# Optimization experiments

Measured on AMD Instinct MI355X. Metric: run time of the kernel, lower is better.

The kernel has to match this reference:

```python
import jax, jax.numpy as jnp
import numpy as np

LD, LU, N, D_IN, D_OUT, K = 16384, 65536, 8, 256, 128, 3


def setup_inputs() -> dict:
    key = jax.random.key(0)
    ks = jax.random.split(key, 7)
    down_features = jax.random.normal(ks[0], (LD, N, D_IN), dtype=jnp.float32)
    up_features = jax.random.normal(ks[1], (LU, N, D_OUT), dtype=jnp.float32)
    idx = jax.random.randint(ks[2], (LU, N, K), 0, LD, dtype=jnp.int32)
    W1 = jax.random.normal(ks[3], (D_IN, D_OUT), dtype=jnp.float32) / np.sqrt(D_IN)
    b1 = jnp.zeros((D_OUT,), dtype=jnp.float32)
    W2 = jax.random.normal(ks[4], (D_OUT, D_OUT), dtype=jnp.float32) / np.sqrt(D_OUT)
    b2 = jnp.zeros((D_OUT,), dtype=jnp.float32)
    return {"down_features": down_features, "up_features": up_features, "idx": idx,
            "W1": W1, "b1": b1, "W2": W2, "b2": b2}


def reference(down_features, up_features, idx, W1, b1, W2, b2):
    # MLP: Linear(d, d_out) -> ReLU -> Linear(d_out, d_out), applied per point
    h = jax.nn.relu(jnp.einsum("lnd,de->lne", down_features, W1) + b1)
    h = jnp.einsum("lnd,de->lne", h, W2) + b2            # (Ld, N, Du)
    # KNN upsample: gather K neighbors per upsampled point, average, residual add
    n = jnp.arange(h.shape[1])[None, :, None]            # (1, N, 1) batch index
    gathered = h[idx, n, :]                              # (Lu, N, K, Du)
    up = up_features + gathered.mean(axis=2)             # (Lu, N, Du)
    return up
```

## Files before the change

kernel.cpp:

```cpp
#include <hip/hip_runtime.h>

#define LD_   16384
#define LU_   65536
#define N_    8
#define DIN   256
#define DOUT  128
#define K_    3
#define M_    (LD_ * N_)

typedef short bf16x8 __attribute__((ext_vector_type(8)));
typedef float f32x4  __attribute__((ext_vector_type(4)));
typedef unsigned int u32x2 __attribute__((ext_vector_type(2)));

__device__ __forceinline__ unsigned short f2bf(float f) {
    unsigned int x = __float_as_uint(f);
    x += 0x7fffu + ((x >> 16) & 1u);
    return (unsigned short)(x >> 16);
}

__device__ __forceinline__ bf16x8 ld_bf16x8(const unsigned short* p) {
    const short4 lo = *(const short4*)p;
    const short4 hi = *(const short4*)(p + 4);
    bf16x8 r = {lo.x, lo.y, lo.z, lo.w, hi.x, hi.y, hi.z, hi.w};
    return r;
}

#define W1_STRIDE 264
#define W2_STRIDE 132
#define H1_STRIDE 132

__global__ __launch_bounds__(512, 2) void knn_mlp_mfma(
    const float* __restrict__ down, const float* __restrict__ W1,
    const float* __restrict__ b1,   const float* __restrict__ W2,
    const float* __restrict__ b2,   unsigned short* __restrict__ h)
{
    __shared__ unsigned short sW1t[DOUT * W1_STRIDE];
    __shared__ unsigned short sW2t[DOUT * W2_STRIDE];
    __shared__ unsigned short sH[8][16 * H1_STRIDE];
    __shared__ float sB1[DOUT], sB2[DOUT];

    const int tid  = threadIdx.x;
    const int wave = tid >> 6, lane = tid & 63;
    const int lm = lane & 15, lg = lane >> 4;

    const int row0 = blockIdx.x * 512 + wave * 16;
    const float* dbase = down + (size_t)(row0 + lm) * DIN + lg * 8;

    float4 raw[16];
    #pragma unroll
    for (int k = 0; k < 8; ++k) {
        raw[2 * k]     = *(const float4*)(dbase + k * 32);
        raw[2 * k + 1] = *(const float4*)(dbase + k * 32 + 4);
    }

    #pragma unroll
    for (int it = 0; it < 16; ++it) {
        const int fid = it * 512 + tid;
        const int k = fid >> 5, n4 = (fid & 31) * 4;
        const float4 w = ((const float4*)W1)[fid];
        sW1t[(n4 + 0) * W1_STRIDE + k] = f2bf(w.x);
        sW1t[(n4 + 1) * W1_STRIDE + k] = f2bf(w.y);
        sW1t[(n4 + 2) * W1_STRIDE + k] = f2bf(w.z);
        sW1t[(n4 + 3) * W1_STRIDE + k] = f2bf(w.w);
    }
    #pragma unroll
    for (int it = 0; it < 8; ++it) {
        const int fid = it * 512 + tid;
        const int k = fid >> 5, n4 = (fid & 31) * 4;
        const float4 w = ((const float4*)W2)[fid];
        sW2t[(n4 + 0) * W2_STRIDE + k] = f2bf(w.x);
        sW2t[(n4 + 1) * W2_STRIDE + k] = f2bf(w.y);
        sW2t[(n4 + 2) * W2_STRIDE + k] = f2bf(w.z);
        sW2t[(n4 + 3) * W2_STRIDE + k] = f2bf(w.w);
    }
    if (tid < 32)                 ((float4*)sB1)[tid]      = ((const float4*)b1)[tid];
    else if (tid < 64)            ((float4*)sB2)[tid - 32] = ((const float4*)b2)[tid - 32];
    __syncthreads();

    unsigned short* hw = sH[wave];

    #pragma unroll
    for (int pass = 0; pass < 4; ++pass) {
        const int chunk = row0 + pass * 128;

        bf16x8 A[8];
        #pragma unroll
        for (int k = 0; k < 8; ++k) {
            const float4 r0 = raw[2 * k], r1 = raw[2 * k + 1];
            const bf16x8 a = {(short)f2bf(r0.x), (short)f2bf(r0.y), (short)f2bf(r0.z), (short)f2bf(r0.w),
                              (short)f2bf(r1.x), (short)f2bf(r1.y), (short)f2bf(r1.z), (short)f2bf(r1.w)};
            A[k] = a;
        }

        if (pass < 3) {
            const float* dp = dbase + (size_t)(pass + 1) * 128 * DIN;
            #pragma unroll
            for (int k = 0; k < 8; ++k) {
                raw[2 * k]     = *(const float4*)(dp + k * 32);
                raw[2 * k + 1] = *(const float4*)(dp + k * 32 + 4);
            }
        }

        f32x4 acc[8];
        #pragma unroll
        for (int nt = 0; nt < 8; ++nt) acc[nt] = (f32x4){0.f, 0.f, 0.f, 0.f};
        #pragma unroll
        for (int k = 0; k < 8; ++k) {
            const int koff = k * 32 + lg * 8;
            #pragma unroll
            for (int nt = 0; nt < 8; ++nt) {
                const bf16x8 Wf = ld_bf16x8(&sW1t[(nt * 16 + lm) * W1_STRIDE + koff]);
                acc[nt] = __builtin_amdgcn_mfma_f32_16x16x32_bf16(Wf, A[k], acc[nt], 0, 0, 0);
            }
        }

        #pragma unroll
        for (int nt = 0; nt < 8; ++nt) {
            const float4 bq = *(const float4*)&sB1[nt * 16 + lg * 4];
            ushort4 st;
            st.x = f2bf(fmaxf(acc[nt][0] + bq.x, 0.0f));
            st.y = f2bf(fmaxf(acc[nt][1] + bq.y, 0.0f));
            st.z = f2bf(fmaxf(acc[nt][2] + bq.z, 0.0f));
            st.w = f2bf(fmaxf(acc[nt][3] + bq.w, 0.0f));
            *(ushort4*)&hw[lm * H1_STRIDE + nt * 16 + lg * 4] = st;
        }
        asm volatile("s_waitcnt lgkmcnt(0)" ::: "memory");

        f32x4 acc2[8];
        #pragma unroll
        for (int nt = 0; nt < 8; ++nt) acc2[nt] = (f32x4){0.f, 0.f, 0.f, 0.f};
        #pragma unroll
        for (int ks = 0; ks < 4; ++ks) {
            const int koff = ks * 32 + lg * 8;
            const bf16x8 Bh = ld_bf16x8(&hw[lm * H1_STRIDE + koff]);
            #pragma unroll
            for (int nt = 0; nt < 8; ++nt) {
                const bf16x8 Wf = ld_bf16x8(&sW2t[(nt * 16 + lm) * W2_STRIDE + koff]);
                acc2[nt] = __builtin_amdgcn_mfma_f32_16x16x32_bf16(Wf, Bh, acc2[nt], 0, 0, 0);
            }
        }

        #pragma unroll
        for (int nt = 0; nt < 8; ++nt) {
            const float4 bq = *(const float4*)&sB2[nt * 16 + lg * 4];
            ushort4 st;
            st.x = f2bf(acc2[nt][0] + bq.x);
            st.y = f2bf(acc2[nt][1] + bq.y);
            st.z = f2bf(acc2[nt][2] + bq.z);
            st.w = f2bf(acc2[nt][3] + bq.w);
            *(ushort4*)&h[(size_t)(chunk + lm) * DOUT + nt * 16 + lg * 4] = st;
        }
    }
}

__global__ __launch_bounds__(256) void knn_gather(
    const float* __restrict__ up, const int* __restrict__ idx,
    const unsigned int* __restrict__ h32, float* __restrict__ out)
{
    const int wave = threadIdx.x >> 6, lane = threadIdx.x & 63;
    const int half = lane >> 5, lih = lane & 31;
    const long long wid  = (long long)blockIdx.x * 4 + wave;
    const long long base = wid * 64;

    const int* ip = idx + (base + lane) * 3;
    const int mi0 = ip[0], mi1 = ip[1], mi2 = ip[2];

    const u32x2* hg   = (const u32x2*)h32;
    const f32x4* upv  = (const f32x4*)up;
    f32x4*       outv = (f32x4*)out;

    #pragma unroll
    for (int gb = 0; gb < 8; ++gb) {
        u32x2 ga[4][3];
        f32x4 uu[4];
        int   pp[4];
        #pragma unroll
        for (int u = 0; u < 4; ++u) {
            const int p = (gb * 4 + u) * 2 + half;
            pp[u] = p;
            const int i0 = __shfl(mi0, p);
            const int i1 = __shfl(mi1, p);
            const int i2 = __shfl(mi2, p);
            const int n  = p & 7;
            ga[u][0] = hg[(unsigned)(i0 * 8 + n) * 32u + lih];
            ga[u][1] = hg[(unsigned)(i1 * 8 + n) * 32u + lih];
            ga[u][2] = hg[(unsigned)(i2 * 8 + n) * 32u + lih];
            uu[u] = __builtin_nontemporal_load(&upv[(base + p) * 32 + lih]);
        }
        #pragma unroll
        for (int u = 0; u < 4; ++u) {
            float s0 = 0.f, s1 = 0.f, s2 = 0.f, s3 = 0.f;
            #pragma unroll
            for (int j = 0; j < 3; ++j) {
                const u32x2 v = ga[u][j];
                s0 += __uint_as_float(v.x << 16);
                s1 += __uint_as_float(v.x & 0xffff0000u);
                s2 += __uint_as_float(v.y << 16);
                s3 += __uint_as_float(v.y & 0xffff0000u);
            }
            f32x4 o;
            o.x = uu[u].x + s0 * (1.0f / 3.0f);
            o.y = uu[u].y + s1 * (1.0f / 3.0f);
            o.z = uu[u].z + s2 * (1.0f / 3.0f);
            o.w = uu[u].w + s3 * (1.0f / 3.0f);
            __builtin_nontemporal_store(o, &outv[(base + pp[u]) * 32 + lih]);
        }
    }
}

extern "C" void kernel_launch(void* const* d_in, const int* in_sizes, int n_in,
                              void* d_out, int out_size, void* d_ws, size_t ws_size,
                              hipStream_t stream)
{
    const float* down = (const float*)d_in[0];
    const float* up   = (const float*)d_in[1];
    const int*   idx  = (const int*)d_in[2];
    const float* W1   = (const float*)d_in[3];
    const float* b1   = (const float*)d_in[4];
    const float* W2   = (const float*)d_in[5];
    const float* b2   = (const float*)d_in[6];
    float* out = (float*)d_out;
    unsigned short* h = (unsigned short*)d_ws;

    knn_mlp_mfma<<<256, 512, 0, stream>>>(down, W1, b1, W2, b2, h);
    knn_gather<<<2048, 256, 0, stream>>>(up, idx, (const unsigned int*)h, out);
}
```

Before: 554.7 us.

## Fuse MLP and KNN gather into one cooperative kernel with grid sync

Merges the MLP kernel and the gather kernel into one cooperative launch of 256 blocks, with a grid-wide barrier between the phases. The gather phase is remapped so each wave handles four 64-point sub-batches in a loop. The intent is to remove the second kernel launch and its inter-kernel gap. The cost is that the gather phase runs with only 256 blocks of 512 threads, far fewer than the original 2048 blocks, which may reduce memory-level parallelism. It also adds the grid sync overhead and requires cooperative launch support.

```diff
diff --git a/kernel.cpp b/kernel.cpp
--- a/kernel.cpp
+++ b/kernel.cpp
@@ -1,4 +1,5 @@
 #include <hip/hip_runtime.h>
+#include <hip/hip_cooperative_groups.h>
 
 #define LD_   16384
 #define LU_   65536
@@ -29,10 +30,12 @@
 #define W2_STRIDE 132
 #define H1_STRIDE 132
 
-__global__ __launch_bounds__(512, 2) void knn_mlp_mfma(
+__global__ __launch_bounds__(512, 2) void knn_fused(
     const float* __restrict__ down, const float* __restrict__ W1,
     const float* __restrict__ b1,   const float* __restrict__ W2,
-    const float* __restrict__ b2,   unsigned short* __restrict__ h)
+    const float* __restrict__ b2,   const float* __restrict__ up,
+    const int* __restrict__ idx,    unsigned short* __restrict__ h,
+    float* __restrict__ out)
 {
     __shared__ unsigned short sW1t[DOUT * W1_STRIDE];
     __shared__ unsigned short sW2t[DOUT * W2_STRIDE];
@@ -43,167 +46,170 @@
     const int wave = tid >> 6, lane = tid & 63;
     const int lm = lane & 15, lg = lane >> 4;
 
-    const int row0 = blockIdx.x * 512 + wave * 16;
-    const float* dbase = down + (size_t)(row0 + lm) * DIN + lg * 8;
-
-    float4 raw[16];
-    #pragma unroll
-    for (int k = 0; k < 8; ++k) {
-        raw[2 * k]     = *(const float4*)(dbase + k * 32);
-        raw[2 * k + 1] = *(const float4*)(dbase + k * 32 + 4);
+    {
+        const int row0 = blockIdx.x * 512 + wave * 16;
+        const float* dbase = down + (size_t)(row0 + lm) * DIN + lg * 8;
+
+        float4 raw[16];
+        #pragma unroll
+        for (int k = 0; k < 8; ++k) {
+            raw[2 * k]     = *(const float4*)(dbase + k * 32);
+            raw[2 * k + 1] = *(const float4*)(dbase + k * 32 + 4);
+        }
+
+        #pragma unroll
+        for (int it = 0; it < 16; ++it) {
+            const int fid = it * 512 + tid;
+            const int k = fid >> 5, n4 = (fid & 31) * 4;
+            const float4 w = ((const float4*)W1)[fid];
+            sW1t[(n4 + 0) * W1_STRIDE + k] = f2bf(w.x);
+            sW1t[(n4 + 1) * W1_STRIDE + k] = f2bf(w.y);
+            sW1t[(n4 + 2) * W1_STRIDE + k] = f2bf(w.z);
+            sW1t[(n4 + 3) * W1_STRIDE + k] = f2bf(w.w);
+        }
+        #pragma unroll
+        for (int it = 0; it < 8; ++it) {
+            const int fid = it * 512 + tid;
+            const int k = fid >> 5, n4 = (fid & 31) * 4;
+            const float4 w = ((const float4*)W2)[fid];
+            sW2t[(n4 + 0) * W2_STRIDE + k] = f2bf(w.x);
+            sW2t[(n4 + 1) * W2_STRIDE + k] = f2bf(w.y);
+            sW2t[(n4 + 2) * W2_STRIDE + k] = f2bf(w.z);
+            sW2t[(n4 + 3) * W2_STRIDE + k] = f2bf(w.w);
+        }
+        if (tid < 32)      ((float4*)sB1)[tid]      = ((const float4*)b1)[tid];
+        else if (tid < 64) ((float4*)sB2)[tid - 32] = ((const float4*)b2)[tid - 32];
+        __syncthreads();
+
+        unsigned short* hw = sH[wave];
+
+        #pragma unroll
+        for (int pass = 0; pass < 4; ++pass) {
+            const int chunk = row0 + pass * 128;
+
+            bf16x8 A[8];
+            #pragma unroll
+            for (int k = 0; k < 8; ++k) {
+                const float4 r0 = raw[2 * k], r1 = raw[2 * k + 1];
+                const bf16x8 a = {(short)f2bf(r0.x), (short)f2bf(r0.y), (short)f2bf(r0.z), (short)f2bf(r0.w),
+                                  (short)f2bf(r1.x), (short)f2bf(r1.y), (short)f2bf(r1.z), (short)f2bf(r1.w)};
+                A[k] = a;
+            }
+
+            if (pass < 3) {
+                const float* dp = dbase + (size_t)(pass + 1) * 128 * DIN;
+                #pragma unroll
+                for (int k = 0; k < 8; ++k) {
+                    raw[2 * k]     = *(const float4*)(dp + k * 32);
+                    raw[2 * k + 1] = *(const float4*)(dp + k * 32 + 4);
+                }
+            }
+
+            f32x4 acc[8];
+            #pragma unroll
+            for (int nt = 0; nt < 8; ++nt) acc[nt] = (f32x4){0.f, 0.f, 0.f, 0.f};
+            #pragma unroll
+            for (int k = 0; k < 8; ++k) {
+                const int koff = k * 32 + lg * 8;
+                #pragma unroll
+                for (int nt = 0; nt < 8; ++nt) {
+                    const bf16x8 Wf = ld_bf16x8(&sW1t[(nt * 16 + lm) * W1_STRIDE + koff]);
+                    acc[nt] = __builtin_amdgcn_mfma_f32_16x16x32_bf16(Wf, A[k], acc[nt], 0, 0, 0);
+                }
+            }
+
+            #pragma unroll
+            for (int nt = 0; nt < 8; ++nt) {
+                const float4 bq = *(const float4*)&sB1[nt * 16 + lg * 4];
+                ushort4 st;
+                st.x = f2bf(fmaxf(acc[nt][0] + bq.x, 0.0f));
+                st.y = f2bf(fmaxf(acc[nt][1] + bq.y, 0.0f));
+                st.z = f2bf(fmaxf(acc[nt][2] + bq.z, 0.0f));
+                st.w = f2bf(fmaxf(acc[nt][3] + bq.w, 0.0f));
+                *(ushort4*)&hw[lm * H1_STRIDE + nt * 16 + lg * 4] = st;
+            }
+            asm volatile("s_waitcnt lgkmcnt(0)" ::: "memory");
+
+            f32x4 acc2[8];
+            #pragma unroll
+            for (int nt = 0; nt < 8; ++nt) acc2[nt] = (f32x4){0.f, 0.f, 0.f, 0.f};
+            #pragma unroll
+            for (int ks = 0; ks < 4; ++ks) {
+                const int koff = ks * 32 + lg * 8;
+                const bf16x8 Bh = ld_bf16x8(&hw[lm * H1_STRIDE + koff]);
+                #pragma unroll
+                for (int nt = 0; nt < 8; ++nt) {
+                    const bf16x8 Wf = ld_bf16x8(&sW2t[(nt * 16 + lm) * W2_STRIDE + koff]);
+                    acc2[nt] = __builtin_amdgcn_mfma_f32_16x16x32_bf16(Wf, Bh, acc2[nt], 0, 0, 0);
+                }
+            }
+
+            #pragma unroll
+            for (int nt = 0; nt < 8; ++nt) {
+                const float4 bq = *(const float4*)&sB2[nt * 16 + lg * 4];
+                ushort4 st;
+                st.x = f2bf(acc2[nt][0] + bq.x);
+                st.y = f2bf(acc2[nt][1] + bq.y);
+                st.z = f2bf(acc2[nt][2] + bq.z);
+                st.w = f2bf(acc2[nt][3] + bq.w);
+                *(ushort4*)&h[(size_t)(chunk + lm) * DOUT + nt * 16 + lg * 4] = st;
+            }
+        }
     }
 
-    #pragma unroll
-    for (int it = 0; it < 16; ++it) {
-        const int fid = it * 512 + tid;
-        const int k = fid >> 5, n4 = (fid & 31) * 4;
-        const float4 w = ((const float4*)W1)[fid];
-        sW1t[(n4 + 0) * W1_STRIDE + k] = f2bf(w.x);
-        sW1t[(n4 + 1) * W1_STRIDE + k] = f2bf(w.y);
-        sW1t[(n4 + 2) * W1_STRIDE + k] = f2bf(w.z);
-        sW1t[(n4 + 3) * W1_STRIDE + k] = f2bf(w.w);
-    }
-    #pragma unroll
-    for (int it = 0; it < 8; ++it) {
-        const int fid = it * 512 + tid;
-        const int k = fid >> 5, n4 = (fid & 31) * 4;
-        const float4 w = ((const float4*)W2)[fid];
-        sW2t[(n4 + 0) * W2_STRIDE + k] = f2bf(w.x);
-        sW2t[(n4 + 1) * W2_STRIDE + k] = f2bf(w.y);
-        sW2t[(n4 + 2) * W2_STRIDE + k] = f2bf(w.z);
-        sW2t[(n4 + 3) * W2_STRIDE + k] = f2bf(w.w);
-    }
-    if (tid < 32)                 ((float4*)sB1)[tid]      = ((const float4*)b1)[tid];
-    else if (tid < 64)            ((float4*)sB2)[tid - 32] = ((const float4*)b2)[tid - 32];
-    __syncthreads();
-
-    unsigned short* hw = sH[wave];
-
-    #pragma unroll
-    for (int pass = 0; pass < 4; ++pass) {
-        const int chunk = row0 + pass * 128;
-
-        bf16x8 A[8];
-        #pragma unroll
-        for (int k = 0; k < 8; ++k) {
-            const float4 r0 = raw[2 * k], r1 = raw[2 * k + 1];
-            const bf16x8 a = {(short)f2bf(r0.x), (short)f2bf(r0.y), (short)f2bf(r0.z), (short)f2bf(r0.w),
-                              (short)f2bf(r1.x), (short)f2bf(r1.y), (short)f2bf(r1.z), (short)f2bf(r1.w)};
-            A[k] = a;
-        }
-
-        if (pass < 3) {
-            const float* dp = dbase + (size_t)(pass + 1) * 128 * DIN;
-            #pragma unroll
-            for (int k = 0; k < 8; ++k) {
-                raw[2 * k]     = *(const float4*)(dp + k * 32);
-                raw[2 * k + 1] = *(const float4*)(dp + k * 32 + 4);
-            }
-        }
-
-        f32x4 acc[8];
-        #pragma unroll
-        for (int nt = 0; nt < 8; ++nt) acc[nt] = (f32x4){0.f, 0.f, 0.f, 0.f};
-        #pragma unroll
-        for (int k = 0; k < 8; ++k) {
-            const int koff = k * 32 + lg * 8;
-            #pragma unroll
-            for (int nt = 0; nt < 8; ++nt) {
-                const bf16x8 Wf = ld_bf16x8(&sW1t[(nt * 16 + lm) * W1_STRIDE + koff]);
-                acc[nt] = __builtin_amdgcn_mfma_f32_16x16x32_bf16(Wf, A[k], acc[nt], 0, 0, 0);
-            }
-        }
-
-        #pragma unroll
-        for (int nt = 0; nt < 8; ++nt) {
-            const float4 bq = *(const float4*)&sB1[nt * 16 + lg * 4];
-            ushort4 st;
-            st.x = f2bf(fmaxf(acc[nt][0] + bq.x, 0.0f));
-            st.y = f2bf(fmaxf(acc[nt][1] + bq.y, 0.0f));
-            st.z = f2bf(fmaxf(acc[nt][2] + bq.z, 0.0f));
-            st.w = f2bf(fmaxf(acc[nt][3] + bq.w, 0.0f));
-            *(ushort4*)&hw[lm * H1_STRIDE + nt * 16 + lg * 4] = st;
-        }
-        asm volatile("s_waitcnt lgkmcnt(0)" ::: "memory");
-
-        f32x4 acc2[8];
-        #pragma unroll
-        for (int nt = 0; nt < 8; ++nt) acc2[nt] = (f32x4){0.f, 0.f, 0.f, 0.f};
-        #pragma unroll
-        for (int ks = 0; ks < 4; ++ks) {
-            const int koff = ks * 32 + lg * 8;
-            const bf16x8 Bh = ld_bf16x8(&hw[lm * H1_STRIDE + koff]);
-            #pragma unroll
-            for (int nt = 0; nt < 8; ++nt) {
-                const bf16x8 Wf = ld_bf16x8(&sW2t[(nt * 16 + lm) * W2_STRIDE + koff]);
-                acc2[nt] = __builtin_amdgcn_mfma_f32_16x16x32_bf16(Wf, Bh, acc2[nt], 0, 0, 0);
-            }
-        }
-
-        #pragma unroll
-        for (int nt = 0; nt < 8; ++nt) {
-            const float4 bq = *(const float4*)&sB2[nt * 16 + lg * 4];
-            ushort4 st;
-            st.x = f2bf(acc2[nt][0] + bq.x);
-            st.y = f2bf(acc2[nt][1] + bq.y);
-            st.z = f2bf(acc2[nt][2] + bq.z);
-            st.w = f2bf(acc2[nt][3] + bq.w);
-            *(ushort4*)&h[(size_t)(chunk + lm) * DOUT + nt * 16 + lg * 4] = st;
-        }
-    }
-}
-
-__global__ __launch_bounds__(256) void knn_gather(
-    const float* __restrict__ up, const int* __restrict__ idx,
-    const unsigned int* __restrict__ h32, float* __restrict__ out)
-{
-    const int wave = threadIdx.x >> 6, lane = threadIdx.x & 63;
-    const int half = lane >> 5, lih = lane & 31;
-    const long long wid  = (long long)blockIdx.x * 4 + wave;
-    const long long base = wid * 64;
-
-    const int* ip = idx + (base + lane) * 3;
-    const int mi0 = ip[0], mi1 = ip[1], mi2 = ip[2];
-
-    const u32x2* hg   = (const u32x2*)h32;
-    const f32x4* upv  = (const f32x4*)up;
-    f32x4*       outv = (f32x4*)out;
-
-    #pragma unroll
-    for (int gb = 0; gb < 8; ++gb) {
-        u32x2 ga[4][3];
-        f32x4 uu[4];
-        int   pp[4];
-        #pragma unroll
-        for (int u = 0; u < 4; ++u) {
-            const int p = (gb * 4 + u) * 2 + half;
-            pp[u] = p;
-            const int i0 = __shfl(mi0, p);
-            const int i1 = __shfl(mi1, p);
-            const int i2 = __shfl(mi2, p);
-            const int n  = p & 7;
-            ga[u][0] = hg[(unsigned)(i0 * 8 + n) * 32u + lih];
-            ga[u][1] = hg[(unsigned)(i1 * 8 + n) * 32u + lih];
-            ga[u][2] = hg[(unsigned)(i2 * 8 + n) * 32u + lih];
-            uu[u] = __builtin_nontemporal_load(&upv[(base + p) * 32 + lih]);
-        }
-        #pragma unroll
-        for (int u = 0; u < 4; ++u) {
-            float s0 = 0.f, s1 = 0.f, s2 = 0.f, s3 = 0.f;
-            #pragma unroll
-            for (int j = 0; j < 3; ++j) {
-                const u32x2 v = ga[u][j];
-                s0 += __uint_as_float(v.x << 16);
-                s1 += __uint_as_float(v.x & 0xffff0000u);
-                s2 += __uint_as_float(v.y << 16);
-                s3 += __uint_as_float(v.y & 0xffff0000u);
-            }
-            f32x4 o;
-            o.x = uu[u].x + s0 * (1.0f / 3.0f);
-            o.y = uu[u].y + s1 * (1.0f / 3.0f);
-            o.z = uu[u].z + s2 * (1.0f / 3.0f);
-            o.w = uu[u].w + s3 * (1.0f / 3.0f);
-            __builtin_nontemporal_store(o, &outv[(base + pp[u]) * 32 + lih]);
+    cooperative_groups::this_grid().sync();
+
+    {
+        const int half = lane >> 5, lih = lane & 31;
+        const u32x2* hg   = (const u32x2*)h;
+        const f32x4* upv  = (const f32x4*)up;
+        f32x4*       outv = (f32x4*)out;
+        const long long wid2 = (long long)blockIdx.x * 8 + wave;
+
+        #pragma unroll 1
+        for (int sb = 0; sb < 4; ++sb) {
+            const long long base = wid2 * 256 + sb * 64;
+
+            const int* ip = idx + (base + lane) * 3;
+            const int mi0 = ip[0], mi1 = ip[1], mi2 = ip[2];
+
+            #pragma unroll
+            for (int gb = 0; gb < 8; ++gb) {
+                u32x2 ga[4][3];
+                f32x4 uu[4];
+                int   pp[4];
+                #pragma unroll
+                for (int u = 0; u < 4; ++u) {
+                    const int p = (gb * 4 + u) * 2 + half;
+                    pp[u] = p;
+                    const int i0 = __shfl(mi0, p);
+                    const int i1 = __shfl(mi1, p);
+                    const int i2 = __shfl(mi2, p);
+                    const int n  = p & 7;
+                    ga[u][0] = hg[(unsigned)(i0 * 8 + n) * 32u + lih];
+                    ga[u][1] = hg[(unsigned)(i1 * 8 + n) * 32u + lih];
+                    ga[u][2] = hg[(unsigned)(i2 * 8 + n) * 32u + lih];
+                    uu[u] = __builtin_nontemporal_load(&upv[(base + p) * 32 + lih]);
+                }
+                #pragma unroll
+                for (int u = 0; u < 4; ++u) {
+                    float s0 = 0.f, s1 = 0.f, s2 = 0.f, s3 = 0.f;
+                    #pragma unroll
+                    for (int j = 0; j < 3; ++j) {
+                        const u32x2 v = ga[u][j];
+                        s0 += __uint_as_float(v.x << 16);
+                        s1 += __uint_as_float(v.x & 0xffff0000u);
+                        s2 += __uint_as_float(v.y << 16);
+                        s3 += __uint_as_float(v.y & 0xffff0000u);
+                    }
+                    f32x4 o;
+                    o.x = uu[u].x + s0 * (1.0f / 3.0f);
+                    o.y = uu[u].y + s1 * (1.0f / 3.0f);
+                    o.z = uu[u].z + s2 * (1.0f / 3.0f);
+                    o.w = uu[u].w + s3 * (1.0f / 3.0f);
+                    __builtin_nontemporal_store(o, &outv[(base + pp[u]) * 32 + lih]);
+                }
+            }
         }
     }
 }
@@ -222,6 +228,9 @@
     float* out = (float*)d_out;
     unsigned short* h = (unsigned short*)d_ws;
 
-    knn_mlp_mfma<<<256, 512, 0, stream>>>(down, W1, b1, W2, b2, h);
-    knn_gather<<<2048, 256, 0, stream>>>(up, idx, (const unsigned int*)h, out);
-}
+    void* args[] = {(void*)&down, (void*)&W1, (void*)&b1, (void*)&W2,
+                    (void*)&b2,   (void*)&up, (void*)&idx, (void*)&h,
+                    (void*)&out};
+    hipLaunchCooperativeKernel((const void*)knn_fused, dim3(256), dim3(512),
+                               args, 0, stream);
+}
```

Measured after the change: 639.4 us. 1.15x slower.
